# Performance work log

Measured on AMD Instinct MI355X. Metric: run time of the kernel, lower is better.

Reference implementation:

```python
import jax, jax.numpy as jnp
import numpy as np


def setup_inputs() -> dict:
    key = jax.random.key(0)
    k1, k2 = jax.random.split(key)
    BN, C, P, K = 1024, 3, 128, 15
    patches = jax.random.normal(k1, (BN, C, P, P), dtype=jnp.float32)
    kernels = jax.random.normal(k2, (BN, C, K, K), dtype=jnp.float32)
    return {
        "patches": patches,
        "kernels": kernels,
        "kernel_size": K,
        "patch_size": P,
        "fft_size": 256,  # unused by the spatial-domain path, kept for interface parity
    }


def reference(patches, kernels, kernel_size, patch_size, fft_size):
    # patches: [BN, C, P, P], kernels: [BN, C, K, K] (C == C_k branch of original)
    BN, C, P, _ = patches.shape
    K = kernel_size
    pad = K // 2
    # torch flips the kernel then runs correlation (F.conv2d) -> true convolution
    kf = jnp.flip(kernels, axis=(-2, -1))
    x = patches.reshape(1, BN * C, P, P)          # one big grouped conv
    w = kf.reshape(BN * C, 1, K, K)               # OIHW, one filter per group
    y = jax.lax.conv_general_dilated(
        x, w,
        window_strides=(1, 1),
        padding=[(pad, pad), (pad, pad)],          # zero pad == F.pad + valid conv
        dimension_numbers=("NCHW", "OIHW", "NCHW"),
        feature_group_count=BN * C,
    )
    return y.reshape(BN, C, P, P)
```

## Files before the change

kernel.cpp:

```cpp
#include <hip/hip_runtime.h>


namespace {

constexpr int P      = 128;
constexpr int K      = 15;
constexpr int HALF   = 64;
constexpr int LROWS  = HALF + K - 1;
constexpr int LM     = 36;
constexpr int LWP    = 160;
constexpr int NT     = 256;

__device__ __forceinline__ int dein(int m) {
    return (m >> 1) + (m & 1) * 20;
}

__device__ __forceinline__ int rowkey(int row) {
    return (row >> 1) & 6;
}

__global__ __launch_bounds__(NT, 3)
void dwconv_kernel(const float* __restrict__ patches,
                   const float* __restrict__ kernels,
                   float* __restrict__ out)
{
    __shared__ float xs[LROWS * LWP];
    __shared__ float ks[K * 16];

    const int tid   = threadIdx.x;
    const int n     = blockIdx.x >> 1;
    const int halfb = blockIdx.x & 1;
    const int ibase = halfb * HALF;

    const float* img  = patches + (size_t)n * (P * P);
    const float* kern = kernels + (size_t)n * (K * K);

    if (tid < K * 16) {
        const int a = tid >> 4;
        const int b = tid & 15;
        ks[tid] = (b < K) ? kern[a * K + b] : 0.0f;
    }

    for (int idx = tid; idx < LROWS * LM; idx += NT) {
        const int row = idx / LM;
        const int m   = idx - row * LM;
        const int r   = ibase - 7 + row;
        const int g0  = m * 4 - 8;
        float4 v = make_float4(0.f, 0.f, 0.f, 0.f);
        if ((unsigned)r < (unsigned)P) {
            if (g0 >= 0 && g0 + 3 < P) {
                v = *reinterpret_cast<const float4*>(img + r * P + g0);
            } else {
                float t0 = 0.f, t1 = 0.f, t2 = 0.f, t3 = 0.f;
                const float* rp = img + r * P;
                if ((unsigned)(g0 + 0) < (unsigned)P) t0 = rp[g0 + 0];
                if ((unsigned)(g0 + 1) < (unsigned)P) t1 = rp[g0 + 1];
                if ((unsigned)(g0 + 2) < (unsigned)P) t2 = rp[g0 + 2];
                if ((unsigned)(g0 + 3) < (unsigned)P) t3 = rp[g0 + 3];
                v = make_float4(t0, t1, t2, t3);
            }
        }
        const int phys = dein(m) ^ rowkey(row);
        *reinterpret_cast<float4*>(xs + row * LWP + 4 * phys) = v;
    }
    __syncthreads();

    const int ty = tid >> 4;
    const int tx = tid & 15;
    const int i0 = ty * 4;
    const int j0 = tx * 8;

    const int dbase[6] = { tx + 0, tx + 20, tx + 1, tx + 21, tx + 2, tx + 22 };

    float acc[4][8];
    #pragma unroll
    for (int rr = 0; rr < 4; ++rr)
        #pragma unroll
        for (int s = 0; s < 8; ++s)
            acc[rr][s] = 0.0f;

    #pragma unroll 1
    for (int a = 0; a < K; ++a) {
        float kv[16];
        #pragma unroll
        for (int q = 0; q < 4; ++q) {
            const float4 kk = *reinterpret_cast<const float4*>(ks + a * 16 + q * 4);
            kv[q * 4 + 0] = kk.x;
            kv[q * 4 + 1] = kk.y;
            kv[q * 4 + 2] = kk.z;
            kv[q * 4 + 3] = kk.w;
        }

        #pragma unroll
        for (int rr = 0; rr < 4; ++rr) {
            const int lrow = i0 + rr + (K - 1) - a;
            const float* xrow = xs + lrow * LWP;
            const int    key  = rowkey(lrow);
            float xw[24];
            #pragma unroll
            for (int q = 0; q < 6; ++q) {
                const float4 xv =
                    *reinterpret_cast<const float4*>(xrow + 4 * (dbase[q] ^ key));
                xw[q * 4 + 0] = xv.x;
                xw[q * 4 + 1] = xv.y;
                xw[q * 4 + 2] = xv.z;
                xw[q * 4 + 3] = xv.w;
            }
            #pragma unroll
            for (int b = 0; b < K; ++b) {
                #pragma unroll
                for (int s = 0; s < 8; ++s) {
                    acc[rr][s] = fmaf(xw[s + 15 - b], kv[b], acc[rr][s]);
                }
            }
        }
    }

    float* orow = out + (size_t)n * (P * P) + (size_t)(ibase + i0) * P + j0;
    #pragma unroll
    for (int rr = 0; rr < 4; ++rr) {
        *reinterpret_cast<float4*>(orow + rr * P + 0) =
            make_float4(acc[rr][0], acc[rr][1], acc[rr][2], acc[rr][3]);
        *reinterpret_cast<float4*>(orow + rr * P + 4) =
            make_float4(acc[rr][4], acc[rr][5], acc[rr][6], acc[rr][7]);
    }
}

}

extern "C" void kernel_launch(void* const* d_in, const int* in_sizes, int n_in,
                              void* d_out, int out_size, void* d_ws, size_t ws_size,
                              hipStream_t stream) {
    const float* patches = (const float*)d_in[0];
    const float* kernels = (const float*)d_in[1];
    float* out = (float*)d_out;

    const int n_images = in_sizes[0] / (P * P);
    const int grid = n_images * 2;

    dwconv_kernel<<<grid, NT, 0, stream>>>(patches, kernels, out);
}
```

Baseline: 600.6 us.

## Reuse each shared-memory input row across four output rows via register rotation

Restructures the convolution loop so each input row is read from shared memory once and applied to all four output rows a thread owns. Kernel rows are held in a rotating four-slot register buffer, with a prologue and epilogue for the edges. Kernel weights are now read directly from global memory, which lets the compiler use uniform scalar loads, and the shared kernel array is removed. This cuts shared-memory reads of the input by about 3x, at the cost of roughly 60 extra registers for kernel values, which could limit occupancy.

```diff
diff --git a/kernel.cpp b/kernel.cpp
--- a/kernel.cpp
+++ b/kernel.cpp
@@ -25,7 +25,6 @@
                    float* __restrict__ out)
 {
     __shared__ float xs[LROWS * LWP];
-    __shared__ float ks[K * 16];
 
     const int tid   = threadIdx.x;
     const int n     = blockIdx.x >> 1;
@@ -34,12 +33,6 @@
 
     const float* img  = patches + (size_t)n * (P * P);
     const float* kern = kernels + (size_t)n * (K * K);
-
-    if (tid < K * 16) {
-        const int a = tid >> 4;
-        const int b = tid & 15;
-        ks[tid] = (b < K) ? kern[a * K + b] : 0.0f;
-    }
 
     for (int idx = tid; idx < LROWS * LM; idx += NT) {
         const int row = idx / LM;
@@ -79,42 +72,60 @@
         for (int s = 0; s < 8; ++s)
             acc[rr][s] = 0.0f;
 
+    float xw[24];
+    float kr[4][K];
+
+    auto loadx = [&](int t) {
+        const int lrow = i0 + t;
+        const float* xrow = xs + lrow * LWP;
+        const int key = rowkey(lrow);
+        #pragma unroll
+        for (int q = 0; q < 6; ++q) {
+            const float4 xv =
+                *reinterpret_cast<const float4*>(xrow + 4 * (dbase[q] ^ key));
+            xw[q * 4 + 0] = xv.x;
+            xw[q * 4 + 1] = xv.y;
+            xw[q * 4 + 2] = xv.z;
+            xw[q * 4 + 3] = xv.w;
+        }
+    };
+
+    auto loadk = [&](int slot, int a) {
+        #pragma unroll
+        for (int b = 0; b < K; ++b) kr[slot][b] = kern[a * K + b];
+    };
+
+    auto fmarow = [&](int rr, int slot) {
+        #pragma unroll
+        for (int b = 0; b < K; ++b)
+            #pragma unroll
+            for (int s = 0; s < 8; ++s)
+                acc[rr][s] = fmaf(xw[s + 15 - b], kr[slot][b], acc[rr][s]);
+    };
+
+    loadk(2, 14); loadk(1, 13); loadk(0, 12);
+    loadx(0); fmarow(0, 2);
+    loadx(1); fmarow(0, 1); fmarow(1, 2);
+    loadx(2); fmarow(0, 0); fmarow(1, 1); fmarow(2, 2);
+
     #pragma unroll 1
-    for (int a = 0; a < K; ++a) {
-        float kv[16];
-        #pragma unroll
-        for (int q = 0; q < 4; ++q) {
-            const float4 kk = *reinterpret_cast<const float4*>(ks + a * 16 + q * 4);
-            kv[q * 4 + 0] = kk.x;
-            kv[q * 4 + 1] = kk.y;
-            kv[q * 4 + 2] = kk.z;
-            kv[q * 4 + 3] = kk.w;
-        }
+    for (int tb = 3; tb <= 14; tb += 4) {
+        loadk(3, 14 - tb); loadx(tb + 0);
+        fmarow(0, 3); fmarow(1, 0); fmarow(2, 1); fmarow(3, 2);
 
-        #pragma unroll
-        for (int rr = 0; rr < 4; ++rr) {
-            const int lrow = i0 + rr + (K - 1) - a;
-            const float* xrow = xs + lrow * LWP;
-            const int    key  = rowkey(lrow);
-            float xw[24];
-            #pragma unroll
-            for (int q = 0; q < 6; ++q) {
-                const float4 xv =
-                    *reinterpret_cast<const float4*>(xrow + 4 * (dbase[q] ^ key));
-                xw[q * 4 + 0] = xv.x;
-                xw[q * 4 + 1] = xv.y;
-                xw[q * 4 + 2] = xv.z;
-                xw[q * 4 + 3] = xv.w;
-            }
-            #pragma unroll
-            for (int b = 0; b < K; ++b) {
-                #pragma unroll
-                for (int s = 0; s < 8; ++s) {
-                    acc[rr][s] = fmaf(xw[s + 15 - b], kv[b], acc[rr][s]);
-                }
-            }
-        }
+        loadk(2, 13 - tb); loadx(tb + 1);
+        fmarow(0, 2); fmarow(1, 3); fmarow(2, 0); fmarow(3, 1);
+
+        loadk(1, 12 - tb); loadx(tb + 2);
+        fmarow(0, 1); fmarow(1, 2); fmarow(2, 3); fmarow(3, 0);
+
+        loadk(0, 11 - tb); loadx(tb + 3);
+        fmarow(0, 0); fmarow(1, 1); fmarow(2, 2); fmarow(3, 3);
     }
+
+    loadx(15); fmarow(1, 0); fmarow(2, 1); fmarow(3, 2);
+    loadx(16); fmarow(2, 0); fmarow(3, 1);
+    loadx(17); fmarow(3, 0);
 
     float* orow = out + (size_t)n * (P * P) + (size_t)(ibase + i0) * P + j0;
     #pragma unroll
```

New measurement: 490.0 us. 1.23x faster.
